# Performance work log

Hardware: AMD Instinct MI355X
Metric: run time of the kernel (lower is better)

The kernel has to match this reference:

```python
import jax, jax.numpy as jnp
import numpy as np

N_TYPES = 4  # global / and / or / leaf node types (indep_weights)


def gcn_layer(x, W_stack, b, edge_src, edge_dst, edge_w, labels, num_nodes):
    # Per-node-type dense projection: compute all 4 projections, then select by label.
    # all4: [4, N, out]
    all4 = jnp.einsum('nd,kdo->kno', x, W_stack)
    support = jnp.take_along_axis(all4, labels[None, :, None].astype(jnp.int32), axis=0)[0]  # [N, out]
    # Sparse adjacency propagation: out[dst] += w * support[src]  (torch.spmm equivalent)
    msgs = support[edge_src] * edge_w[:, None]  # [E, out]
    agg = jax.ops.segment_sum(msgs, edge_dst, num_segments=num_nodes)
    return agg + b


def setup_inputs() -> dict:
    key = jax.random.key(0)
    ks = jax.random.split(key, 12)
    N, E = 50000, 1600000
    nfeat, nhid, nclass = 256, 256, 64
    x = jax.random.normal(ks[0], (N, nfeat), dtype=jnp.float32)
    edge_src = jax.random.randint(ks[1], (E,), 0, N, dtype=jnp.int32)
    edge_dst = jax.random.randint(ks[2], (E,), 0, N, dtype=jnp.int32)
    edge_w = jax.random.uniform(ks[3], (E,), dtype=jnp.float32)
    labels = jax.random.randint(ks[4], (N,), 0, N_TYPES, dtype=jnp.int32)
    def winit(k, fi, fo):
        s = 1.0 / np.sqrt(fo)
        return jax.random.uniform(k, (N_TYPES, fi, fo), minval=-s, maxval=s, dtype=jnp.float32)
    def binit(k, fo):
        s = 1.0 / np.sqrt(fo)
        return jax.random.uniform(k, (fo,), minval=-s, maxval=s, dtype=jnp.float32)
    return {
        'x': x, 'edge_src': edge_src, 'edge_dst': edge_dst, 'edge_w': edge_w, 'labels': labels,
        'W1': winit(ks[5], nfeat, nhid), 'b1': binit(ks[6], nhid),
        'W2': winit(ks[7], nhid, nhid), 'b2': binit(ks[8], nhid),
        'W3': winit(ks[9], nhid, nclass), 'b3': binit(ks[10], nclass),
    }


def reference(x, edge_src, edge_dst, edge_w, labels, W1, b1, W2, b2, W3, b3):
    N = x.shape[0]
    h = jax.nn.relu(gcn_layer(x, W1, b1, edge_src, edge_dst, edge_w, labels, N))
    # F.dropout with p=0 (module default) is identity
    h = jax.nn.relu(gcn_layer(h, W2, b2, edge_src, edge_dst, edge_w, labels, N))
    out = gcn_layer(h, W3, b3, edge_src, edge_dst, edge_w, labels, N)
    return out
```

## Files before the change

kernel.cpp:

```cpp
#include <hip/hip_runtime.h>
#include <hip/hip_bf16.h>

#define NT 4
#define FEAT 256
#define OUT3 64

typedef __bf16 bf16x8 __attribute__((ext_vector_type(8)));
typedef float  f32x4  __attribute__((ext_vector_type(4)));

__device__ inline unsigned int f2bf_bits(float f) {
    __hip_bfloat16 h = __float2bfloat16(f);
    unsigned short u;
    __builtin_memcpy(&u, &h, 2);
    return (unsigned int)u;
}
__device__ inline float bfl(unsigned int u) { return __uint_as_float(u << 16); }
__device__ inline float bfh(unsigned int u) { return __uint_as_float(u & 0xffff0000u); }
__device__ __host__ inline int nat_of(int p) {
    int lo = p & 63;
    return (p & ~63) | (((lo & 3) << 4) | (lo >> 2));
}

__global__ __launch_bounds__(512) void pass_a(const int* __restrict__ dst,
                                              const int* __restrict__ labels,
                                              int* __restrict__ bcnt, int* __restrict__ lc,
                                              int E, int N) {
    __shared__ int h[256];
    __shared__ int lh[NT];
    int tid = threadIdx.x;
    if (tid < 256) h[tid] = 0;
    if (tid < NT) lh[tid] = 0;
    __syncthreads();
    int base = blockIdx.x * 4096;
#pragma unroll
    for (int k = 0; k < 8; ++k) {
        int e = base + k * 512 + tid;
        if (e < E) atomicAdd(&h[((unsigned)dst[e]) >> 8], 1);
    }
#pragma unroll
    for (int k = 0; k < 8; ++k) {
        int i = base + k * 512 + tid;
        if (i < N) atomicAdd(&lh[labels[i]], 1);
    }
    __syncthreads();
    if (tid < 256) { int v = h[tid]; if (v) atomicAdd(&bcnt[tid], v); }
    if (tid < NT) { int v = lh[tid]; if (v) atomicAdd(&lc[tid], v); }
}

__global__ __launch_bounds__(256) void scan_master(
    const int* __restrict__ bcnt, const int* __restrict__ lc,
    int* __restrict__ boff, int* __restrict__ gcur, int* __restrict__ rb,
    int* __restrict__ lstart, int NB, int N, int E) {
    __shared__ int s[256];
    int tid = threadIdx.x;
    int own = (tid < NB) ? bcnt[tid] : 0;
    s[tid] = own;
    __syncthreads();
    for (int d = 1; d < 256; d <<= 1) {
        int v = (tid >= d) ? s[tid - d] : 0;
        __syncthreads();
        s[tid] += v;
        __syncthreads();
    }
    int excl = s[tid] - own;
    if (tid < NB) { boff[tid] = excl; gcur[tid] = excl; }
    if (tid == 0) {
        boff[NB] = E; rb[(size_t)N * 8] = E;
        int run = 0;
        for (int l = 0; l < NT; ++l) {
            lstart[l] = run;
            run += (lc[l] + 63) & ~63;
        }
    }
}

__global__ void scatter_nodes(const int* __restrict__ labels, const int* __restrict__ lstart,
                              int* __restrict__ lcur, int* __restrict__ iperm, int N) {
    int n = blockIdx.x * 256 + threadIdx.x;
    int lab = (n < N) ? labels[n] : -1;
    int lane = threadIdx.x & 63;
    for (int l = 0; l < NT; ++l) {
        unsigned long long m = __ballot(lab == l);
        if (m == 0ull) continue;
        int leader = __builtin_ctzll(m);
        int base = 0;
        if (lane == leader) base = atomicAdd(&lcur[l], (int)__popcll(m));
        base = __shfl(base, leader, 64);
        if (lab == l) {
            int prefix = (int)__popcll(m & ((1ull << lane) - 1ull));
            iperm[n] = lstart[l] + base + prefix;
        }
    }
}

__global__ __launch_bounds__(512) void fuse_a(
    const int* __restrict__ src, const int* __restrict__ dst, const float* __restrict__ w,
    const int* __restrict__ iperm, int* __restrict__ gcur, uint2* __restrict__ earr, int E,
    const float* __restrict__ x, unsigned short* __restrict__ actLo,
    unsigned short* __restrict__ actHi, int total4,
    const float* __restrict__ W1, const float* __restrict__ W2, const float* __restrict__ W3,
    const float* __restrict__ b1, const float* __restrict__ b2,
    unsigned short* __restrict__ W1b, unsigned short* __restrict__ W2b,
    unsigned short* __restrict__ W3b, float* __restrict__ biasPerm,
    int nbEB, int nbX) {
    int tid = threadIdx.x;
    int blk = (int)blockIdx.x;
    if (blk < nbEB) {
        __shared__ int h[256];
        __shared__ int basearr[256];
        if (tid < 256) h[tid] = 0;
        __syncthreads();
        int base = blk * 4096;
        int b[8], rank[8], px[8]; float wv[8];
#pragma unroll
        for (int k = 0; k < 8; ++k) {
            int e = base + k * 512 + tid;
            if (e < E) {
                int d = dst[e];
                b[k] = ((unsigned)d) >> 8;
                px[k] = iperm[src[e]] | ((d & 255) << 16);
                wv[k] = w[e];
                rank[k] = atomicAdd(&h[b[k]], 1);
            } else b[k] = -1;
        }
        __syncthreads();
        if (tid < 256) { int c = h[tid]; basearr[tid] = c ? atomicAdd(&gcur[tid], c) : 0; }
        __syncthreads();
#pragma unroll
        for (int k = 0; k < 8; ++k) {
            if (b[k] >= 0) {
                int pos = basearr[b[k]] + rank[k];
                earr[pos] = make_uint2((unsigned)px[k], __float_as_uint(wv[k]));
            }
        }
    } else if (blk < nbEB + nbX) {
        int i = (blk - nbEB) * 512 + tid;
        if (i < total4) {
            float4 v = ((const float4*)x)[i];
            unsigned int lo = f2bf_bits(v.x) | (f2bf_bits(v.y) << 16);
            unsigned int hi = f2bf_bits(v.z) | (f2bf_bits(v.w) << 16);
            int slot = iperm[i >> 6];
            unsigned short* dp = ((i & 63) >= 32) ? actHi : actLo;
            ((uint2*)dp)[(size_t)slot * 32 + (i & 31)] = make_uint2(lo, hi);
        }
    } else {
        const int S = NT * FEAT * FEAT;
        const int S3 = NT * FEAT * OUT3;
        int idx = (blk - nbEB - nbX) * 512 + tid;
        if (idx < 2 * S + S3) {
            const float* W; unsigned short* D; int OUTF; int t; bool remap;
            if (idx < S)          { W = W1; D = W1b; OUTF = FEAT; t = idx;         remap = false; }
            else if (idx < 2 * S) { W = W2; D = W2b; OUTF = FEAT; t = idx - S;     remap = true; }
            else                  { W = W3; D = W3b; OUTF = OUT3; t = idx - 2 * S; remap = true; }
            int n = t % OUTF;
            int r = t / OUTF;
            int j = r & 7, q = (r >> 3) & 3, k0 = (r >> 5) & 7, lab = r >> 8;
            int k_slot = k0 * 32 + q * 8 + j;
            int k_src = remap ? nat_of(k_slot) : k_slot;
            float f = W[((size_t)(lab * FEAT + k_src)) * OUTF + n];
            D[(((size_t)lab * 8 + k0) * OUTF + n) * 32 + q * 8 + j] = (unsigned short)f2bf_bits(f);
        } else {
            int p2 = idx - (2 * S + S3);
            if (p2 < 256) biasPerm[p2] = b1[nat_of(p2)];
            else if (p2 < 512) biasPerm[p2] = b2[nat_of(p2 - 256)];
        }
    }
}

__device__ void bucket_sort_body(int b, const uint2* __restrict__ earr,
                                 const int* __restrict__ boff, int* __restrict__ rb,
                                 unsigned int* __restrict__ edata, int N) {
    int s = boff[b], e = boff[b + 1];
    __shared__ int cnt[2048], off[2048], ts[256];
    int tid = threadIdx.x;
#pragma unroll
    for (int k = 0; k < 8; ++k) cnt[tid * 8 + k] = 0;
    __syncthreads();
    for (int i = s + tid; i < e; i += 256) {
        unsigned int xx = earr[i].x;
        int key = (((xx >> 16) & 255) << 3) | ((xx & 0xffffu) >> 13);
        atomicAdd(&cnt[key], 1);
    }
    __syncthreads();
    int run = 0;
#pragma unroll
    for (int k = 0; k < 8; ++k) { off[tid * 8 + k] = run; run += cnt[tid * 8 + k]; }
    ts[tid] = run;
    __syncthreads();
    int own = ts[tid];
    for (int d = 1; d < 256; d <<= 1) {
        int v = (tid >= d) ? ts[tid - d] : 0;
        __syncthreads();
        ts[tid] += v;
        __syncthreads();
    }
    int texcl = ts[tid] - own;
#pragma unroll
    for (int k = 0; k < 8; ++k) off[tid * 8 + k] += texcl;
    __syncthreads();
    int node = b * 256 + tid;
    if (node < N) {
#pragma unroll
        for (int k = 0; k < 8; ++k) rb[(size_t)node * 8 + k] = s + off[tid * 8 + k];
    }
    __syncthreads();
    for (int i = s + tid; i < e; i += 256) {
        uint2 r = earr[i];
        unsigned int xx = r.x;
        int key = (((xx >> 16) & 255) << 3) | ((xx & 0xffffu) >> 13);
        int k = atomicAdd(&off[key], 1);
        edata[s + k] = (f2bf_bits(__uint_as_float(r.y)) << 16) | (xx & 0xffffu);
    }
}

__device__ void proj256_body(int gb,
                             const unsigned short* __restrict__ actLo,
                             const unsigned short* __restrict__ actHi,
                             const unsigned short* __restrict__ Wswz,
                             const int* __restrict__ lstart,
                             unsigned short* __restrict__ supLo,
                             unsigned short* __restrict__ supHi) {
    int warp = threadIdx.x >> 6;
    int lane = threadIdx.x & 63;
    int m0 = gb * 64;
    int lab = (m0 >= lstart[1]) + (m0 >= lstart[2]) + (m0 >= lstart[3]);
    int q = lane >> 4, c = lane & 15;
    int n0 = warp * 64;

    const unsigned short* aLo = actLo + (size_t)(m0 + c) * 128 + q * 8;
    const unsigned short* aHi = actHi + (size_t)(m0 + c) * 128 + q * 8;
    const unsigned short* bb = Wswz + (size_t)lab * FEAT * 256 + (size_t)(n0 + c) * 32 + q * 8;

    f32x4 acc[4][4] = {};
#pragma unroll
    for (int k0 = 0; k0 < 8; ++k0) {
        const unsigned short* abase = (k0 < 4) ? aLo : aHi;
        int koff = (k0 & 3) * 32;
        bf16x8 a[4];
#pragma unroll
        for (int t = 0; t < 4; ++t) a[t] = *(const bf16x8*)(abase + (size_t)t * 2048 + koff);
        const unsigned short* bk = bb + (size_t)k0 * 32 * 256;
#pragma unroll
        for (int u = 0; u < 4; ++u) {
            bf16x8 bfrag = *(const bf16x8*)(bk + u * 512);
#pragma unroll
            for (int t = 0; t < 4; ++t)
                acc[t][u] = __builtin_amdgcn_mfma_f32_16x16x32_bf16(a[t], bfrag, acc[t][u], 0, 0, 0);
        }
    }
    uint2* ov = (uint2*)((n0 >= 128) ? supHi : supLo);
    int cix = ((n0 & 64) >> 2) + c;
#pragma unroll
    for (int t = 0; t < 4; ++t) {
#pragma unroll
        for (int r = 0; r < 4; ++r) {
            int row = m0 + t * 16 + q * 4 + r;
            unsigned int lo = f2bf_bits(acc[t][0][r]) | (f2bf_bits(acc[t][1][r]) << 16);
            unsigned int hi = f2bf_bits(acc[t][2][r]) | (f2bf_bits(acc[t][3][r]) << 16);
            ov[(size_t)row * 32 + cix] = make_uint2(lo, hi);
        }
    }
}

__global__ __launch_bounds__(256) void fuse_b(
    const uint2* __restrict__ earr, const int* __restrict__ boff,
    int* __restrict__ rb, unsigned int* __restrict__ edata, int N, int NB,
    const unsigned short* __restrict__ actLo, const unsigned short* __restrict__ actHi,
    const unsigned short* __restrict__ Wswz, const int* __restrict__ lstart,
    unsigned short* __restrict__ supLo, unsigned short* __restrict__ supHi) {
    int blk = (int)blockIdx.x;
    if (blk < NB) bucket_sort_body(blk, earr, boff, rb, edata, N);
    else proj256_body(blk - NB, actLo, actHi, Wswz, lstart, supLo, supHi);
}

__global__ __launch_bounds__(256) void proj256_kernel(
    const unsigned short* __restrict__ actLo, const unsigned short* __restrict__ actHi,
    const unsigned short* __restrict__ Wswz, const int* __restrict__ lstart,
    unsigned short* __restrict__ supLo, unsigned short* __restrict__ supHi) {
    proj256_body((int)blockIdx.x, actLo, actHi, Wswz, lstart, supLo, supHi);
}

__global__ __launch_bounds__(256) void proj64_kernel(
    const unsigned short* __restrict__ actLo, const unsigned short* __restrict__ actHi,
    const unsigned short* __restrict__ Wswz, const int* __restrict__ lstart,
    unsigned short* __restrict__ outp) {
    int warp = threadIdx.x >> 6;
    int lane = threadIdx.x & 63;
    int m0 = blockIdx.x * 64;
    int lab = (m0 >= lstart[1]) + (m0 >= lstart[2]) + (m0 >= lstart[3]);
    int q = lane >> 4, c = lane & 15;
    int mb = m0 + warp * 16;

    const unsigned short* aLo = actLo + (size_t)(mb + c) * 128 + q * 8;
    const unsigned short* aHi = actHi + (size_t)(mb + c) * 128 + q * 8;
    const unsigned short* bb = Wswz + (size_t)lab * FEAT * OUT3 + (size_t)c * 32 + q * 8;

    f32x4 acc[4] = {};
#pragma unroll
    for (int k0 = 0; k0 < 8; ++k0) {
        const unsigned short* abase = (k0 < 4) ? aLo : aHi;
        bf16x8 a = *(const bf16x8*)(abase + (k0 & 3) * 32);
        const unsigned short* bk = bb + (size_t)k0 * 32 * OUT3;
#pragma unroll
        for (int u = 0; u < 4; ++u) {
            bf16x8 bfrag = *(const bf16x8*)(bk + u * 512);
            acc[u] = __builtin_amdgcn_mfma_f32_16x16x32_bf16(a, bfrag, acc[u], 0, 0, 0);
        }
    }
    uint2* ov = (uint2*)outp;
#pragma unroll
    for (int r = 0; r < 4; ++r) {
        int row = mb + q * 4 + r;
        unsigned int lo = f2bf_bits(acc[0][r]) | (f2bf_bits(acc[1][r]) << 16);
        unsigned int hi = f2bf_bits(acc[2][r]) | (f2bf_bits(acc[3][r]) << 16);
        ov[(size_t)row * 16 + c] = make_uint2(lo, hi);
    }
}

__global__ __launch_bounds__(256) void agg256x_kernel(
    const unsigned int* __restrict__ supLo, const unsigned int* __restrict__ supHi,
    const int* __restrict__ rb, const unsigned int* __restrict__ edata,
    const int* __restrict__ iperm, const float* __restrict__ biasPerm, int bOff,
    unsigned int* __restrict__ outLo, unsigned int* __restrict__ outHi, int N) {
    int blk = (int)blockIdx.x;
    int half = blk & 1;
    int warp = __builtin_amdgcn_readfirstlane((int)(threadIdx.x >> 6));
    int node = (blk >> 1) * 4 + warp;
    if (node >= N) return;
    int lane = threadIdx.x & 63;
    const unsigned int* sup = half ? supHi : supLo;
    unsigned int* outp = half ? outHi : outLo;
    int s = __builtin_amdgcn_readfirstlane(rb[(size_t)node * 8]);
    int e = __builtin_amdgcn_readfirstlane(rb[(size_t)node * 8 + 8]);
    int slot = __builtin_amdgcn_readfirstlane(iperm[node]);
    float a0 = 0.f, a1 = 0.f;
    int j = s;
    for (; j + 16 <= e; j += 16) {
        unsigned int ed[16], v[16];
#pragma unroll
        for (int u = 0; u < 16; ++u) ed[u] = edata[j + u];
        __builtin_amdgcn_sched_barrier(0);
#pragma unroll
        for (int u = 0; u < 16; ++u) v[u] = sup[(size_t)(ed[u] & 0xffff) * 64 + lane];
        __builtin_amdgcn_sched_barrier(0);
#pragma unroll
        for (int u = 0; u < 16; ++u) {
            float w = __uint_as_float(ed[u] & 0xffff0000u);
            a0 += w * bfl(v[u]); a1 += w * bfh(v[u]);
        }
    }
    if (j < e) {
        unsigned int ed[16], v[16]; float wm[16];
#pragma unroll
        for (int u = 0; u < 16; ++u) {
            int jj = j + u;
            int jc = (jj < e) ? jj : e - 1;
            ed[u] = edata[jc];
            wm[u] = (jj < e) ? __uint_as_float(ed[u] & 0xffff0000u) : 0.f;
        }
        __builtin_amdgcn_sched_barrier(0);
#pragma unroll
        for (int u = 0; u < 16; ++u) v[u] = sup[(size_t)(ed[u] & 0xffff) * 64 + lane];
        __builtin_amdgcn_sched_barrier(0);
#pragma unroll
        for (int u = 0; u < 16; ++u) { a0 += wm[u] * bfl(v[u]); a1 += wm[u] * bfh(v[u]); }
    }
    float2 b = ((const float2*)(biasPerm + bOff + half * 128))[lane];
    a0 = fmaxf(a0 + b.x, 0.f);
    a1 = fmaxf(a1 + b.y, 0.f);
    unsigned int o = f2bf_bits(a0) | (f2bf_bits(a1) << 16);
    __builtin_nontemporal_store(o, &outp[(size_t)slot * 64 + lane]);
}

__global__ __launch_bounds__(256) void agg64_kernel(
    const unsigned short* __restrict__ sup, const int* __restrict__ rb,
    const unsigned int* __restrict__ edata, const float* __restrict__ b3,
    float* __restrict__ outp, int N) {
    int warp = __builtin_amdgcn_readfirstlane((int)(threadIdx.x >> 6));
    int node = (int)blockIdx.x * 4 + warp;
    if (node >= N) return;
    int lane = threadIdx.x & 63;
    int s = __builtin_amdgcn_readfirstlane(rb[(size_t)node * 8]);
    int e = __builtin_amdgcn_readfirstlane(rb[(size_t)node * 8 + 8]);
    float a = 0.f;
    int j = s;
    for (; j + 16 <= e; j += 16) {
        unsigned int ed[16]; unsigned short v[16];
#pragma unroll
        for (int u = 0; u < 16; ++u) ed[u] = edata[j + u];
#pragma unroll
        for (int u = 0; u < 16; ++u) v[u] = sup[(size_t)(ed[u] & 0xffff) * 64 + lane];
#pragma unroll
        for (int u = 0; u < 16; ++u)
            a += __uint_as_float(ed[u] & 0xffff0000u) * __uint_as_float((unsigned int)v[u] << 16);
    }
    if (j < e) {
        unsigned int ed[16]; float wm[16]; unsigned short v[16];
#pragma unroll
        for (int u = 0; u < 16; ++u) {
            int jj = j + u;
            int jc = (jj < e) ? jj : e - 1;
            ed[u] = edata[jc];
            wm[u] = (jj < e) ? __uint_as_float(ed[u] & 0xffff0000u) : 0.f;
        }
#pragma unroll
        for (int u = 0; u < 16; ++u) v[u] = sup[(size_t)(ed[u] & 0xffff) * 64 + lane];
#pragma unroll
        for (int u = 0; u < 16; ++u)
            a += wm[u] * __uint_as_float((unsigned int)v[u] << 16);
    }
    int natp = (((lane & 3) << 4) | (lane >> 2));
    outp[(size_t)node * 64 + natp] = a + b3[natp];
}

extern "C" void kernel_launch(void* const* d_in, const int* in_sizes, int n_in,
                              void* d_out, int out_size, void* d_ws, size_t ws_size,
                              hipStream_t stream) {
    const float* x        = (const float*)d_in[0];
    const int*   edge_src = (const int*)d_in[1];
    const int*   edge_dst = (const int*)d_in[2];
    const float* edge_w   = (const float*)d_in[3];
    const int*   labels   = (const int*)d_in[4];
    const float* W1 = (const float*)d_in[5];
    const float* b1 = (const float*)d_in[6];
    const float* W2 = (const float*)d_in[7];
    const float* b2 = (const float*)d_in[8];
    const float* W3 = (const float*)d_in[9];
    const float* b3 = (const float*)d_in[10];

    const int N = in_sizes[0] / FEAT;
    const int E = in_sizes[1];
    const int NB = (N + 255) >> 8;
    const int G64 = (N + NT * 64 + 63) / 64;
    const int slotCap = G64 * 64;

    char* p = (char*)d_ws;
    auto alloc = [&](size_t bytes) -> char* {
        char* r = p;
        p += (bytes + 255) & ~(size_t)255;
        return r;
    };
    unsigned short* bufA = (unsigned short*)alloc((size_t)slotCap * FEAT * 2);
    unsigned short* bufB = (unsigned short*)alloc((size_t)slotCap * FEAT * 2);
    unsigned short* W1b  = (unsigned short*)alloc((size_t)NT * FEAT * FEAT * 2);
    unsigned short* W2b  = (unsigned short*)alloc((size_t)NT * FEAT * FEAT * 2);
    unsigned short* W3b  = (unsigned short*)alloc((size_t)NT * FEAT * OUT3 * 2);
    float*        biasPerm = (float*)alloc(512 * 4);
    int*          rb     = (int*)alloc(((size_t)N * 8 + 8) * 4);
    unsigned int* edata  = (unsigned int*)alloc((size_t)E * 4);
    int*          iperm  = (int*)alloc((size_t)N * 4);
    int*          counters = (int*)alloc(264 * 4);
    int*          boff   = (int*)alloc(257 * 4);
    int*          gcur   = (int*)alloc(256 * 4);
    int*          lstart = (int*)alloc(64);
    int* bcnt = counters;
    int* lc   = counters + 256;
    int* lcur = counters + 260;

    unsigned short* actLo = bufA;
    unsigned short* actHi = bufA + (size_t)slotCap * 128;
    unsigned short* supLo = bufB;
    unsigned short* supHi = bufB + (size_t)slotCap * 128;
    uint2* earr = (uint2*)d_out;

    const int nbEB = (E + 4095) / 4096;
    const int total4 = N * 64;
    const int nbX = (total4 + 511) / 512;
    const int totW = 2 * NT * FEAT * FEAT + NT * FEAT * OUT3 + 512;
    const int nbW = (totW + 511) / 512;

    hipMemsetAsync(counters, 0, 264 * 4, stream);
    pass_a<<<nbEB, 512, 0, stream>>>(edge_dst, labels, bcnt, lc, E, N);
    scan_master<<<1, 256, 0, stream>>>(bcnt, lc, boff, gcur, rb, lstart, NB, N, E);
    scatter_nodes<<<(N + 255) / 256, 256, 0, stream>>>(labels, lstart, lcur, iperm, N);
    fuse_a<<<nbEB + nbX + nbW, 512, 0, stream>>>(
        edge_src, edge_dst, edge_w, iperm, gcur, earr, E,
        x, actLo, actHi, total4,
        W1, W2, W3, b1, b2, W1b, W2b, W3b, biasPerm, nbEB, nbX);

    const int aggGrid = (N + 3) / 4;
    fuse_b<<<NB + G64, 256, 0, stream>>>(earr, boff, rb, edata, N, NB,
                                         actLo, actHi, W1b, lstart, supLo, supHi);
    agg256x_kernel<<<2 * aggGrid, 256, 0, stream>>>(
        (const unsigned int*)supLo, (const unsigned int*)supHi, rb, edata, iperm,
        biasPerm, 0, (unsigned int*)actLo, (unsigned int*)actHi, N);
    proj256_kernel<<<G64, 256, 0, stream>>>(actLo, actHi, W2b, lstart, supLo, supHi);
    agg256x_kernel<<<2 * aggGrid, 256, 0, stream>>>(
        (const unsigned int*)supLo, (const unsigned int*)supHi, rb, edata, iperm,
        biasPerm, 256, (unsigned int*)actLo, (unsigned int*)actHi, N);
    proj64_kernel<<<G64, 256, 0, stream>>>(actLo, actHi, W3b, lstart, bufB);
    agg64_kernel<<<aggGrid, 256, 0, stream>>>(bufB, rb, edata, b3, (float*)d_out, N);
}
```

Before: 475.0 us.

## Process source-index bands across 13 nodes per wave in 256-wide aggregation

```diff
diff --git a/kernel.cpp b/kernel.cpp
--- a/kernel.cpp
+++ b/kernel.cpp
@@ -4,6 +4,8 @@
 #define NT 4
 #define FEAT 256
 #define OUT3 64
+#define NPW 13
+#define NBANDA 4
 
 typedef __bf16 bf16x8 __attribute__((ext_vector_type(8)));
 typedef float  f32x4  __attribute__((ext_vector_type(4)));
@@ -317,7 +319,7 @@
     }
 }
 
-__global__ __launch_bounds__(256) void agg256x_kernel(
+__global__ __launch_bounds__(256) void agg256b_kernel(
     const unsigned int* __restrict__ supLo, const unsigned int* __restrict__ supHi,
     const int* __restrict__ rb, const unsigned int* __restrict__ edata,
     const int* __restrict__ iperm, const float* __restrict__ biasPerm, int bOff,
@@ -325,51 +327,68 @@
     int blk = (int)blockIdx.x;
     int half = blk & 1;
     int warp = __builtin_amdgcn_readfirstlane((int)(threadIdx.x >> 6));
-    int node = (blk >> 1) * 4 + warp;
-    if (node >= N) return;
+    int wid = (blk >> 1) * 4 + warp;
+    int n0 = wid * NPW;
+    if (n0 >= N) return;
     int lane = threadIdx.x & 63;
     const unsigned int* sup = half ? supHi : supLo;
     unsigned int* outp = half ? outHi : outLo;
-    int s = __builtin_amdgcn_readfirstlane(rb[(size_t)node * 8]);
-    int e = __builtin_amdgcn_readfirstlane(rb[(size_t)node * 8 + 8]);
-    int slot = __builtin_amdgcn_readfirstlane(iperm[node]);
-    float a0 = 0.f, a1 = 0.f;
-    int j = s;
-    for (; j + 16 <= e; j += 16) {
-        unsigned int ed[16], v[16];
-#pragma unroll
-        for (int u = 0; u < 16; ++u) ed[u] = edata[j + u];
-        __builtin_amdgcn_sched_barrier(0);
-#pragma unroll
-        for (int u = 0; u < 16; ++u) v[u] = sup[(size_t)(ed[u] & 0xffff) * 64 + lane];
-        __builtin_amdgcn_sched_barrier(0);
-#pragma unroll
-        for (int u = 0; u < 16; ++u) {
-            float w = __uint_as_float(ed[u] & 0xffff0000u);
-            a0 += w * bfl(v[u]); a1 += w * bfh(v[u]);
-        }
-    }
-    if (j < e) {
-        unsigned int ed[16], v[16]; float wm[16];
-#pragma unroll
-        for (int u = 0; u < 16; ++u) {
-            int jj = j + u;
-            int jc = (jj < e) ? jj : e - 1;
-            ed[u] = edata[jc];
-            wm[u] = (jj < e) ? __uint_as_float(ed[u] & 0xffff0000u) : 0.f;
-        }
-        __builtin_amdgcn_sched_barrier(0);
-#pragma unroll
-        for (int u = 0; u < 16; ++u) v[u] = sup[(size_t)(ed[u] & 0xffff) * 64 + lane];
-        __builtin_amdgcn_sched_barrier(0);
-#pragma unroll
-        for (int u = 0; u < 16; ++u) { a0 += wm[u] * bfl(v[u]); a1 += wm[u] * bfh(v[u]); }
+    float a0[NPW], a1[NPW];
+#pragma unroll
+    for (int t = 0; t < NPW; ++t) { a0[t] = 0.f; a1[t] = 0.f; }
+    for (int bd = 0; bd < NBANDA; ++bd) {
+#pragma unroll
+        for (int t = 0; t < NPW; ++t) {
+            int n = n0 + t;
+            if (n >= N) continue;
+            int j  = __builtin_amdgcn_readfirstlane(rb[(size_t)n * 8 + bd * 2]);
+            int j1 = __builtin_amdgcn_readfirstlane(rb[(size_t)n * 8 + bd * 2 + 2]);
+            float aa0 = a0[t], aa1 = a1[t];
+            for (; j + 8 <= j1; j += 8) {
+                unsigned int ed[8], v[8];
+#pragma unroll
+                for (int u = 0; u < 8; ++u) ed[u] = edata[j + u];
+                __builtin_amdgcn_sched_barrier(0);
+#pragma unroll
+                for (int u = 0; u < 8; ++u) v[u] = sup[(size_t)(ed[u] & 0xffff) * 64 + lane];
+                __builtin_amdgcn_sched_barrier(0);
+#pragma unroll
+                for (int u = 0; u < 8; ++u) {
+                    float w = __uint_as_float(ed[u] & 0xffff0000u);
+                    aa0 += w * bfl(v[u]); aa1 += w * bfh(v[u]);
+                }
+            }
+            if (j < j1) {
+                unsigned int ed[8], v[8]; float wm[8];
+#pragma unroll
+                for (int u = 0; u < 8; ++u) {
+                    int jj = j + u;
+                    int jc = (jj < j1) ? jj : j1 - 1;
+                    ed[u] = edata[jc];
+                    wm[u] = (jj < j1) ? __uint_as_float(ed[u] & 0xffff0000u) : 0.f;
+                }
+                __builtin_amdgcn_sched_barrier(0);
+#pragma unroll
+                for (int u = 0; u < 8; ++u) v[u] = sup[(size_t)(ed[u] & 0xffff) * 64 + lane];
+                __builtin_amdgcn_sched_barrier(0);
+#pragma unroll
+                for (int u = 0; u < 8; ++u) { aa0 += wm[u] * bfl(v[u]); aa1 += wm[u] * bfh(v[u]); }
+            }
+            a0[t] = aa0; a1[t] = aa1;
+        }
     }
     float2 b = ((const float2*)(biasPerm + bOff + half * 128))[lane];
-    a0 = fmaxf(a0 + b.x, 0.f);
-    a1 = fmaxf(a1 + b.y, 0.f);
-    unsigned int o = f2bf_bits(a0) | (f2bf_bits(a1) << 16);
-    __builtin_nontemporal_store(o, &outp[(size_t)slot * 64 + lane]);
+#pragma unroll
+    for (int t = 0; t < NPW; ++t) {
+        int n = n0 + t;
+        if (n < N) {
+            int slot = __builtin_amdgcn_readfirstlane(iperm[n]);
+            float r0 = fmaxf(a0[t] + b.x, 0.f);
+            float r1 = fmaxf(a1[t] + b.y, 0.f);
+            unsigned int o = f2bf_bits(r0) | (f2bf_bits(r1) << 16);
+            __builtin_nontemporal_store(o, &outp[(size_t)slot * 64 + lane]);
+        }
+    }
 }
 
 __global__ __launch_bounds__(256) void agg64_kernel(
@@ -478,14 +497,16 @@
         x, actLo, actHi, total4,
         W1, W2, W3, b1, b2, W1b, W2b, W3b, biasPerm, nbEB, nbX);
 
+    const int wavesP = (N + NPW - 1) / NPW;
+    const int blkP   = (wavesP + 3) / 4;
     const int aggGrid = (N + 3) / 4;
     fuse_b<<<NB + G64, 256, 0, stream>>>(earr, boff, rb, edata, N, NB,
                                          actLo, actHi, W1b, lstart, supLo, supHi);
-    agg256x_kernel<<<2 * aggGrid, 256, 0, stream>>>(
+    agg256b_kernel<<<2 * blkP, 256, 0, stream>>>(
         (const unsigned int*)supLo, (const unsigned int*)supHi, rb, edata, iperm,
         biasPerm, 0, (unsigned int*)actLo, (unsigned int*)actHi, N);
     proj256_kernel<<<G64, 256, 0, stream>>>(actLo, actHi, W2b, lstart, supLo, supHi);
-    agg256x_kernel<<<2 * aggGrid, 256, 0, stream>>>(
+    agg256b_kernel<<<2 * blkP, 256, 0, stream>>>(
         (const unsigned int*)supLo, (const unsigned int*)supHi, rb, edata, iperm,
         biasPerm, 256, (unsigned int*)actLo, (unsigned int*)actHi, N);
     proj64_kernel<<<G64, 256, 0, stream>>>(actLo, actHi, W3b, lstart, bufB);
```

New measurement: 596.2 us. 1.26x slower.
